# Kernel optimization log

Hardware: AMD Instinct MI355X
Metric: run time of the kernel (lower is better)

Reference implementation:

```python
import jax, jax.numpy as jnp
from jax import lax
import numpy as np

B = 65536
DIM_OBS = 9
DIM_ACT = 4
H = 192
DN = ('NCHW', 'OIHW', 'NCHW')


def _conv(x, w, stride):
    return lax.conv_general_dilated(x, w, (stride, stride), 'VALID', dimension_numbers=DN)


def setup_inputs() -> dict:
    key = jax.random.key(0)
    ks = jax.random.split(key, 16)
    n = lambda k, shp, s: (jax.random.normal(k, shp, dtype=jnp.float32) * s)
    inp = {
        'x': n(ks[0], (B, 1, 12, 16), 1.0),
        'v': n(ks[1], (B, DIM_OBS), 1.0),
        'hx': n(ks[2], (B, H), 1.0),
        # stem convs (no bias)
        'w1': n(ks[3], (32, 1, 2, 2), 0.5),
        'w2': n(ks[4], (64, 32, 3, 3), 0.06),
        'w3': n(ks[5], (128, 64, 3, 3), 0.04),
        'w_stem': n(ks[6], (H, 128 * 2 * 4), 0.03),   # Linear(1024, 192, bias=False)
        # v_proj (weight scaled by 0.5 as in __init__)
        'w_vproj': n(ks[7], (H, DIM_OBS), 0.5 / np.sqrt(DIM_OBS)),
        'b_vproj': n(ks[8], (H,), 0.1),
        # GRUCell(192, 192): gate order r, z, n
        'w_ih': n(ks[9], (3 * H, H), 1.0 / np.sqrt(H)),
        'w_hh': n(ks[10], (3 * H, H), 1.0 / np.sqrt(H)),
        'b_ih': n(ks[11], (3 * H,), 0.05),
        'b_hh': n(ks[12], (3 * H,), 0.05),
        # fc (weight scaled by 0.01 as in __init__)
        'w_fc': n(ks[13], (DIM_ACT, H), 0.01 / np.sqrt(H)),
    }
    return inp


def reference(x, v, hx, w1, w2, w3, w_stem, w_vproj, b_vproj,
              w_ih, w_hh, b_ih, b_hh, w_fc):
    lrelu = lambda t: jax.nn.leaky_relu(t, 0.05)
    # vision stem: [B,1,12,16] -> [B,32,6,8] -> [B,64,4,6] -> [B,128,2,4]
    h = lrelu(_conv(x, w1, 2))
    h = lrelu(_conv(h, w2, 1))
    h = lrelu(_conv(h, w3, 1))
    img_feat = h.reshape(h.shape[0], -1) @ w_stem.T          # [B,192]
    state_feat = v @ w_vproj.T + b_vproj                      # [B,192]
    fused = lrelu(img_feat + state_feat)
    # GRUCell (torch gate order: r, z, n)
    gi = fused @ w_ih.T + b_ih                                # [B,576]
    gh = hx @ w_hh.T + b_hh                                   # [B,576]
    ir, iz, i_n = jnp.split(gi, 3, axis=-1)
    hr, hz, h_n = jnp.split(gh, 3, axis=-1)
    r = jax.nn.sigmoid(ir + hr)
    z = jax.nn.sigmoid(iz + hz)
    n = jnp.tanh(i_n + r * h_n)
    hx_new = (1.0 - z) * n + z * hx
    act = lrelu(hx_new) @ w_fc.T                              # [B,4]
    return act, hx_new
```

## Files before the change

### kernel.cpp

```cpp
#include <hip/hip_runtime.h>


typedef short bf8 __attribute__((ext_vector_type(8)));
typedef float f4  __attribute__((ext_vector_type(4)));

#define MFMA(a, b, c) __builtin_amdgcn_mfma_f32_16x16x32_bf16(a, b, c, 0, 0, 0)

#define W3_OFF    18432
#define WSTEM_OFF 92160
#define WIH_OFF   294912
#define WHH_OFF   405504
#define W_TOTAL   516096
#define C3_OFF    (1 << 20)
#define C2Q_OFF   68157440

__device__ __forceinline__ unsigned short f2bf(float f) {
    unsigned int u = __float_as_uint(f);
    u += 0x7fffu + ((u >> 16) & 1u);
    return (unsigned short)(u >> 16);
}
__device__ __forceinline__ float bf2f(unsigned short h) {
    return __uint_as_float(((unsigned int)h) << 16);
}
__device__ __forceinline__ float lrelu(float v) { return v > 0.f ? v : 0.05f * v; }
__device__ __forceinline__ float sigm(float x) { return 1.f / (1.f + __expf(-x)); }
__device__ __forceinline__ float tanh_(float x) {
    float e = __expf(2.f * x);
    return 1.f - 2.f / (e + 1.f);
}

__global__ void prep_weights(const float* __restrict__ w2, const float* __restrict__ w3,
                             const float* __restrict__ wstem, const float* __restrict__ wvp,
                             const float* __restrict__ wih, const float* __restrict__ whh,
                             unsigned short* __restrict__ o) {
    int i = blockIdx.x * 256 + threadIdx.x;
    if (i >= W_TOTAL) return;
    float val;
    if (i < W3_OFF) {
        int n = i / 288, k = i - n * 288;
        val = w2[n * 288 + (k & 31) * 9 + (k >> 5)];
    } else if (i < WSTEM_OFF) {
        int d = i - W3_OFF;
        int n = d / 576, k = d - n * 576;
        val = w3[n * 576 + (k & 63) * 9 + (k >> 6)];
    } else if (i < WIH_OFF) {
        int d = i - WSTEM_OFF;
        int n = d / 1056, k = d - n * 1056;
        if (k < 1024)       val = wstem[(n << 10) + (k & 127) * 8 + (k >> 7)];
        else if (k < 1033)  val = wvp[n * 9 + (k - 1024)];
        else                val = 0.f;
    } else if (i < WHH_OFF) {
        val = wih[i - WIH_OFF];
    } else {
        val = whh[i - WHH_OFF];
    }
    o[i] = f2bf(val);
}

__global__ __launch_bounds__(256, 2) void conv12(
    const float* __restrict__ x, const float* __restrict__ w1,
    const unsigned short* __restrict__ ws, unsigned short* __restrict__ c2q,
    int sbase)
{
    __shared__ __align__(16) unsigned short lds[6144];
    const int tid = threadIdx.x;
    const int wave = tid >> 6, lane = tid & 63;
    const int col = lane & 15, quad = lane >> 4;
    const int W0 = blockIdx.x * 32;

    bf8 Bf2[9];
    int kq2[9];
    #pragma unroll
    for (int ks = 0; ks < 9; ++ks) {
        int k0 = ks * 32 + quad * 8;
        Bf2[ks] = *(const bf8*)(ws + (wave * 16 + col) * 288 + k0);
        int ky = k0 / 96, r = k0 - 96 * ky;
        kq2[ks] = (ky * 8 + (r >> 5)) * 32 + (r & 31);
    }
    const int g = wave * 2 + (col >> 3);

    for (int c = 0; c < 8; ++c) {
        if (tid < 192) {
            int s = tid / 48, p = tid - s * 48;
            int y = p >> 3, xx = p & 7;
            const float* xp = x + (size_t)(sbase + W0 + c * 4 + s) * 192 + y * 32 + xx * 2;
            float x00 = xp[0], x01 = xp[1], x10 = xp[16], x11 = xp[17];
            int base = s * 1536, sw = (s & 3) << 3;
            #pragma unroll
            for (int cc = 0; cc < 32; ++cc) {
                int co = (cc + p) & 31;
                float a = x00 * w1[co * 4] + x01 * w1[co * 4 + 1]
                        + x10 * w1[co * 4 + 2] + x11 * w1[co * 4 + 3];
                lds[base + ((p * 32 + co) ^ sw)] = f2bf(lrelu(a));
            }
        }
        __syncthreads();

        #pragma unroll
        for (int mt2 = 0; mt2 < 3; ++mt2) {
            int m0 = mt2 * 32 + col, m1 = m0 + 16;
            int s0 = m0 & 3, p0 = m0 >> 2;
            int s1 = m1 & 3, p1 = m1 >> 2;
            int oy0 = p0 / 6, ox0 = p0 - 6 * oy0;
            int oy1 = p1 / 6, ox1 = p1 - 6 * oy1;
            int b0 = s0 * 1536, qb0 = (oy0 * 8 + ox0) * 32, sw0 = (s0 & 3) << 3;
            int b1 = s1 * 1536, qb1 = (oy1 * 8 + ox1) * 32, sw1 = (s1 & 3) << 3;
            f4 acc0 = {0.f, 0.f, 0.f, 0.f}, acc1 = {0.f, 0.f, 0.f, 0.f};
            #pragma unroll
            for (int ks = 0; ks < 9; ++ks) {
                bf8 a0 = *(const bf8*)&lds[b0 + ((qb0 + kq2[ks]) ^ sw0)];
                bf8 a1 = *(const bf8*)&lds[b1 + ((qb1 + kq2[ks]) ^ sw1)];
                acc0 = MFMA(a0, Bf2[ks], acc0);
                acc1 = MFMA(a1, Bf2[ks], acc1);
            }
            #pragma unroll
            for (int r = 0; r < 4; ++r) {
                int m = mt2 * 32 + quad * 4 + r;
                int s = m & 3, pos = m >> 2;
                int sloc = W0 + c * 4 + s;
                int key = (pos + ((sloc & 1) << 2)) & 7;
                c2q[(size_t)sloc * 1536 + pos * 64 + ((g ^ key) << 3) + (col & 7)]
                    = f2bf(lrelu(acc0[r]));
                m += 16; s = m & 3; pos = m >> 2;
                sloc = W0 + c * 4 + s;
                key = (pos + ((sloc & 1) << 2)) & 7;
                c2q[(size_t)sloc * 1536 + pos * 64 + ((g ^ key) << 3) + (col & 7)]
                    = f2bf(lrelu(acc1[r]));
            }
        }
        __syncthreads();
    }
}

__global__ __launch_bounds__(256, 2) void conv3k(
    const unsigned short* __restrict__ ws, const unsigned short* __restrict__ c2q,
    unsigned short* __restrict__ c3, int sbase)
{
    __shared__ __align__(16) unsigned short lds[12288];
    const int tid = threadIdx.x;
    const int wave = tid >> 6, lane = tid & 63;
    const int col = lane & 15, quad = lane >> 4;
    const int h = blockIdx.x & 1;
    const int Q0 = (blockIdx.x >> 1) * 64;
    const int n_in = h * 64 + wave * 16 + col;

    bf8 Bf3[18];
    #pragma unroll
    for (int ks = 0; ks < 18; ++ks)
        Bf3[ks] = *(const bf8*)(ws + W3_OFF + n_in * 576 + ks * 32 + quad * 8);

    int aoff[18];
    {
        int opos = col & 7;
        int oy = opos >> 2, ox = opos & 3;
        int spar = (col >> 3) & 1;
        #pragma unroll
        for (int ks = 0; ks < 18; ++ks) {
            int k0 = ks * 32 + quad * 8;
            int b = k0 >> 6;
            int ky = b / 3, kx = b - 3 * ky;
            int pos2 = (oy + ky) * 6 + (ox + kx);
            int gg = (k0 & 63) >> 3;
            int key = (pos2 + (spar << 2)) & 7;
            aoff[ks] = pos2 * 64 + ((gg ^ key) << 3);
        }
    }
    const int Gl = h * 8 + wave * 2 + (col >> 3);

    for (int c = 0; c < 8; ++c) {
        const unsigned short* s2 = c2q + (size_t)(Q0 + c * 8) * 1536 + tid * 48;
        #pragma unroll
        for (int i = 0; i < 6; ++i)
            *(bf8*)&lds[tid * 48 + i * 8] = *(const bf8*)(s2 + i * 8);
        __syncthreads();

        f4 acc[4];
        #pragma unroll
        for (int mt = 0; mt < 4; ++mt) acc[mt] = (f4){0.f, 0.f, 0.f, 0.f};
        #pragma unroll
        for (int ks = 0; ks < 18; ++ks) {
            #pragma unroll
            for (int mt = 0; mt < 4; ++mt) {
                int sc = mt * 2 + (col >> 3);
                bf8 a = *(const bf8*)&lds[sc * 1536 + aoff[ks]];
                acc[mt] = MFMA(a, Bf3[ks], acc[mt]);
            }
        }
        #pragma unroll
        for (int mt = 0; mt < 4; ++mt) {
            #pragma unroll
            for (int r = 0; r < 4; ++r) {
                int m = quad * 4 + r;
                int sc = mt * 2 + (m >> 3), opos = m & 7;
                int srow = sbase + Q0 + c * 8 + sc;
                c3[(size_t)srow * 1024 + opos * 128 + ((Gl ^ (srow & 15)) << 3) + (col & 7)]
                    = f2bf(lrelu(acc[mt][r]));
            }
        }
        __syncthreads();
    }
}

__global__ __launch_bounds__(256, 2) void stem_gru(
    const unsigned short* __restrict__ ws, const float* __restrict__ v,
    const float* __restrict__ hx, const float* __restrict__ bvp,
    const float* __restrict__ bih, const float* __restrict__ bhh,
    const float* __restrict__ wfc, float* __restrict__ out)
{
    __shared__ __align__(16) unsigned short lds[28672];
    const int tid = threadIdx.x;
    const int wave = tid >> 6, lane = tid & 63;
    const int col = lane & 15, quad = lane >> 4;
    const int S0 = blockIdx.x * 64;
    const unsigned short* c3 = ws + C3_OFF;
    const unsigned short* wstem = ws + WSTEM_OFF;

    f4 acc[4][3];
    #pragma unroll
    for (int mt = 0; mt < 4; ++mt)
        #pragma unroll
        for (int t = 0; t < 3; ++t) acc[mt][t] = (f4){0.f, 0.f, 0.f, 0.f};

    const int sm = tid >> 2, sq = tid & 3;
    const unsigned short* asrc = c3 + (size_t)(S0 + sm) * 1024 + sq * 32;

    #pragma unroll
    for (int i = 0; i < 4; ++i)
        *(bf8*)&lds[12288 + sm * 128 + sq * 32 + i * 8] = *(const bf8*)(asrc + i * 8);
    __syncthreads();

    for (int kc = 0; kc < 8; ++kc) {
        bf8 nx[4];
        if (kc < 7) {
            const unsigned short* s2 = asrc + (kc + 1) * 128;
            #pragma unroll
            for (int i = 0; i < 4; ++i) nx[i] = *(const bf8*)(s2 + i * 8);
        }
        int abase = 12288 + (kc & 1) * 8192;
        #pragma unroll
        for (int ks = 0; ks < 4; ++ks) {
            int kl = ks * 32 + quad * 8;
            int kk = kc * 128 + kl;
            bf8 b0 = *(const bf8*)(wstem + (wave * 48 + col) * 1056 + kk);
            bf8 b1 = *(const bf8*)(wstem + (wave * 48 + 16 + col) * 1056 + kk);
            bf8 b2 = *(const bf8*)(wstem + (wave * 48 + 32 + col) * 1056 + kk);
            #pragma unroll
            for (int mt = 0; mt < 4; ++mt) {
                int m = mt * 16 + col;
                bf8 a = *(const bf8*)&lds[abase + m * 128 + (kl ^ ((m & 15) << 3))];
                acc[mt][0] = MFMA(a, b0, acc[mt][0]);
                acc[mt][1] = MFMA(a, b1, acc[mt][1]);
                acc[mt][2] = MFMA(a, b2, acc[mt][2]);
            }
        }
        if (kc < 7) {
            int wb = 12288 + ((kc + 1) & 1) * 8192;
            #pragma unroll
            for (int i = 0; i < 4; ++i)
                *(bf8*)&lds[wb + sm * 128 + sq * 32 + i * 8] = nx[i];
        }
        __syncthreads();
    }

    if (tid < 64) {
        int m = tid;
        const float* vp = v + (size_t)(S0 + m) * 9;
        __align__(16) unsigned short tmp[32];
        #pragma unroll
        for (int i = 0; i < 9; ++i) tmp[i] = f2bf(vp[i]);
        #pragma unroll
        for (int i = 9; i < 32; ++i) tmp[i] = 0;
        #pragma unroll
        for (int gg = 0; gg < 4; ++gg) {
            int gp = gg ^ (m & 15);
            *(bf8*)&lds[12288 + m * 128 + gp * 8] = *(bf8*)&tmp[gg * 8];
        }
    }
    __syncthreads();
    {
        int kl = quad * 8;
        bf8 b0 = *(const bf8*)(wstem + (wave * 48 + col) * 1056 + 1024 + kl);
        bf8 b1 = *(const bf8*)(wstem + (wave * 48 + 16 + col) * 1056 + 1024 + kl);
        bf8 b2 = *(const bf8*)(wstem + (wave * 48 + 32 + col) * 1056 + 1024 + kl);
        #pragma unroll
        for (int mt = 0; mt < 4; ++mt) {
            int m = mt * 16 + col;
            bf8 a = *(const bf8*)&lds[12288 + m * 128 + (kl ^ ((m & 15) << 3))];
            acc[mt][0] = MFMA(a, b0, acc[mt][0]);
            acc[mt][1] = MFMA(a, b1, acc[mt][1]);
            acc[mt][2] = MFMA(a, b2, acc[mt][2]);
        }
    }

    #pragma unroll
    for (int t = 0; t < 3; ++t) {
        int n = wave * 48 + t * 16 + col;
        float bb = bvp[n];
        #pragma unroll
        for (int mt = 0; mt < 4; ++mt)
            #pragma unroll
            for (int r = 0; r < 4; ++r) {
                int m = mt * 16 + quad * 4 + r;
                lds[m * 192 + (n ^ ((m & 7) << 3))] = f2bf(lrelu(acc[mt][t][r] + bb));
            }
    }
    __syncthreads();

    {
        int m = tid >> 2, qq = tid & 3;
        const float* hp = hx + (size_t)(S0 + m) * 192 + qq * 48;
        #pragma unroll
        for (int i = 0; i < 6; ++i) {
            f4 d = *(const f4*)(hp + i * 8 + 0);
            f4 d2 = *(const f4*)(hp + i * 8 + 4);
            __align__(16) unsigned short tmp[8];
            #pragma unroll
            for (int u = 0; u < 4; ++u) { tmp[u] = f2bf(d[u]); tmp[4 + u] = f2bf(d2[u]); }
            int gg = qq * 6 + i, gp = gg ^ (m & 7);
            *(bf8*)&lds[12288 + m * 192 + gp * 8] = *(bf8*)tmp;
        }
    }
    __syncthreads();

    #pragma unroll
    for (int t = 0; t < 3; ++t) {
        int j0 = (wave * 3 + t) * 16;
        int j = j0 + col;
        const unsigned short* pih = ws + WIH_OFF + j * 192;
        const unsigned short* phh = ws + WHH_OFF + j * 192;
        f4 g0[4], g1[4], g2[4], g3[4], g4[4], g5[4];
        #pragma unroll
        for (int mt = 0; mt < 4; ++mt) {
            g0[mt] = (f4){0.f,0.f,0.f,0.f}; g1[mt] = g0[mt]; g2[mt] = g0[mt];
            g3[mt] = g0[mt]; g4[mt] = g0[mt]; g5[mt] = g0[mt];
        }
        #pragma unroll
        for (int ks = 0; ks < 6; ++ks) {
            int k0 = ks * 32 + quad * 8;
            bf8 bir = *(const bf8*)(pih + k0);
            bf8 bhr = *(const bf8*)(phh + k0);
            bf8 biz = *(const bf8*)(pih + 36864 + k0);
            bf8 bhz = *(const bf8*)(phh + 36864 + k0);
            bf8 bin = *(const bf8*)(pih + 73728 + k0);
            bf8 bhn = *(const bf8*)(phh + 73728 + k0);
            #pragma unroll
            for (int mt = 0; mt < 4; ++mt) {
                int m = mt * 16 + col;
                int off = m * 192 + (k0 ^ ((m & 7) << 3));
                bf8 aF = *(const bf8*)&lds[off];
                bf8 aH = *(const bf8*)&lds[12288 + off];
                g0[mt] = MFMA(aF, bir, g0[mt]);
                g1[mt] = MFMA(aH, bhr, g1[mt]);
                g2[mt] = MFMA(aF, biz, g2[mt]);
                g3[mt] = MFMA(aH, bhz, g3[mt]);
                g4[mt] = MFMA(aF, bin, g4[mt]);
                g5[mt] = MFMA(aH, bhn, g5[mt]);
            }
        }
        float b_ir = bih[j], b_iz = bih[192 + j], b_in = bih[384 + j];
        float b_hr = bhh[j], b_hz = bhh[192 + j], b_hn = bhh[384 + j];
        #pragma unroll
        for (int mt = 0; mt < 4; ++mt)
            #pragma unroll
            for (int r = 0; r < 4; ++r) {
                int s = mt * 16 + quad * 4 + r;
                float rg = sigm(g0[mt][r] + b_ir + g1[mt][r] + b_hr);
                float zg = sigm(g2[mt][r] + b_iz + g3[mt][r] + b_hz);
                float ng = tanh_(g4[mt][r] + b_in + rg * (g5[mt][r] + b_hn));
                float hxv = hx[(size_t)(S0 + s) * 192 + j];
                float hnew = (1.f - zg) * ng + zg * hxv;
                out[65536 * 4 + (size_t)(S0 + s) * 192 + j] = hnew;
            }
    }
    __syncthreads();

    {
        int s = tid & 63, a = tid >> 6;
        const float* hp = out + 65536 * 4 + (size_t)(S0 + s) * 192;
        const float* wf = wfc + a * 192;
        float sum = 0.f;
        #pragma unroll 4
        for (int jj = 0; jj < 48; ++jj) {
            f4 hv = *(const f4*)(hp + jj * 4);
            f4 wv = *(const f4*)(wf + jj * 4);
            #pragma unroll
            for (int u = 0; u < 4; ++u) sum += lrelu(hv[u]) * wv[u];
        }
        out[(size_t)(S0 + s) * 4 + a] = sum;
    }
}

extern "C" void kernel_launch(void* const* d_in, const int* in_sizes, int n_in,
                              void* d_out, int out_size, void* d_ws, size_t ws_size,
                              hipStream_t stream) {
    const float* x     = (const float*)d_in[0];
    const float* v     = (const float*)d_in[1];
    const float* hx    = (const float*)d_in[2];
    const float* w1    = (const float*)d_in[3];
    const float* w2    = (const float*)d_in[4];
    const float* w3    = (const float*)d_in[5];
    const float* wstem = (const float*)d_in[6];
    const float* wvp   = (const float*)d_in[7];
    const float* bvp   = (const float*)d_in[8];
    const float* wih   = (const float*)d_in[9];
    const float* whh   = (const float*)d_in[10];
    const float* bih   = (const float*)d_in[11];
    const float* bhh   = (const float*)d_in[12];
    const float* wfc   = (const float*)d_in[13];
    unsigned short* wsp = (unsigned short*)d_ws;
    unsigned short* c3  = wsp + C3_OFF;
    unsigned short* c2q = wsp + C2Q_OFF;

    prep_weights<<<2016, 256, 0, stream>>>(w2, w3, wstem, wvp, wih, whh, wsp);
    for (int q = 0; q < 4; ++q) {
        conv12<<<512, 256, 0, stream>>>(x, w1, wsp, c2q, q * 16384);
        conv3k<<<512, 256, 0, stream>>>(wsp, c2q, c3, q * 16384);
    }
    stem_gru<<<1024, 256, 0, stream>>>(wsp, v, hx, bvp, bih, bhh, wfc, (float*)d_out);
}
```

Before: 581.7 us.

## Fuse conv1/conv2/conv3 into one kernel keeping conv2 output in LDS

Merges the conv12 and conv3k kernels into a single convfused kernel. conv2 activations stay in shared memory instead of making a round trip through a global c2q buffer, and the four-way batch-chunked launch loop is removed. Each block handles one output-channel half of conv3, so conv1 and conv2 are computed twice (once by each half-block pair) in exchange for skipping the intermediate global write and read. Separately, stem_gru drops its double-buffered LDS staging to a single buffer with extra barriers so it can raise launch bounds to 3 blocks per CU.

```diff
diff --git a/kernel.cpp b/kernel.cpp
--- a/kernel.cpp
+++ b/kernel.cpp
@@ -12,21 +12,20 @@
 #define WHH_OFF   405504
 #define W_TOTAL   516096
 #define C3_OFF    (1 << 20)
-#define C2Q_OFF   68157440
 
 __device__ __forceinline__ unsigned short f2bf(float f) {
     unsigned int u = __float_as_uint(f);
     u += 0x7fffu + ((u >> 16) & 1u);
     return (unsigned short)(u >> 16);
-}
-__device__ __forceinline__ float bf2f(unsigned short h) {
-    return __uint_as_float(((unsigned int)h) << 16);
 }
 __device__ __forceinline__ float lrelu(float v) { return v > 0.f ? v : 0.05f * v; }
 __device__ __forceinline__ float sigm(float x) { return 1.f / (1.f + __expf(-x)); }
 __device__ __forceinline__ float tanh_(float x) {
     float e = __expf(2.f * x);
     return 1.f - 2.f / (e + 1.f);
+}
+__device__ __forceinline__ int swzC(int q, int s) {
+    return q ^ ((s & 3) << 3) ^ ((q >> 1) & 32);
 }
 
 __global__ void prep_weights(const float* __restrict__ w2, const float* __restrict__ w3,
@@ -57,33 +56,58 @@
     o[i] = f2bf(val);
 }
 
-__global__ __launch_bounds__(256, 2) void conv12(
+__global__ __launch_bounds__(256, 2) void convfused(
     const float* __restrict__ x, const float* __restrict__ w1,
-    const unsigned short* __restrict__ ws, unsigned short* __restrict__ c2q,
-    int sbase)
+    const unsigned short* __restrict__ ws, unsigned short* __restrict__ c3)
 {
-    __shared__ __align__(16) unsigned short lds[6144];
+    __shared__ __align__(16) unsigned short lds[31232];
     const int tid = threadIdx.x;
     const int wave = tid >> 6, lane = tid & 63;
     const int col = lane & 15, quad = lane >> 4;
-    const int W0 = blockIdx.x * 32;
-
-    bf8 Bf2[9];
-    int kq2[9];
-    #pragma unroll
-    for (int ks = 0; ks < 9; ++ks) {
-        int k0 = ks * 32 + quad * 8;
-        Bf2[ks] = *(const bf8*)(ws + (wave * 16 + col) * 288 + k0);
-        int ky = k0 / 96, r = k0 - 96 * ky;
-        kq2[ks] = (ky * 8 + (r >> 5)) * 32 + (r & 31);
-    }
-    const int g = wave * 2 + (col >> 3);
-
-    for (int c = 0; c < 8; ++c) {
+    const int h = blockIdx.x & 1;
+    const int S0 = (blockIdx.x >> 1) * 64;
+    const int q8 = quad * 8;
+
+    {
+        int row = tid >> 2, seg = tid & 3;
+        const unsigned short* src = ws + row * 288 + seg * 72;
+        unsigned short* dst = &lds[12288 + row * 296 + seg * 72];
+        #pragma unroll
+        for (int i = 0; i < 9; ++i)
+            *(bf8*)(dst + i * 8) = *(const bf8*)(src + i * 8);
+    }
+
+    const int n_in = h * 64 + wave * 16 + col;
+    bf8 Bf3[18];
+    #pragma unroll
+    for (int ks = 0; ks < 18; ++ks)
+        Bf3[ks] = *(const bf8*)(ws + W3_OFF + n_in * 576 + ks * 32 + q8);
+
+    const int scm = col & 3;
+    const int bb2 = scm * 1536, sw2 = scm << 3;
+    int qbv[6];
+    #pragma unroll
+    for (int mt = 0; mt < 3; ++mt)
+        #pragma unroll
+        for (int hf = 0; hf < 2; ++hf) {
+            int p = mt * 8 + hf * 4 + (col >> 2);
+            int oy = p / 6, ox = p - 6 * oy;
+            qbv[mt * 2 + hf] = (oy * 8 + ox) * 32;
+        }
+    const int s3 = col & 3;
+    const int p30 = col >> 2, p31 = p30 + 4;
+    const int qb30 = p30 * 64;
+    const int qb31 = (6 + (p31 & 3)) * 64;
+    const int b3 = 6144 + s3 * 1536;
+    const int G = h * 8 + wave * 2 + (col >> 3);
+
+    __syncthreads();
+
+    for (int c = 0; c < 16; ++c) {
         if (tid < 192) {
             int s = tid / 48, p = tid - s * 48;
             int y = p >> 3, xx = p & 7;
-            const float* xp = x + (size_t)(sbase + W0 + c * 4 + s) * 192 + y * 32 + xx * 2;
+            const float* xp = x + (size_t)(S0 + c * 4 + s) * 192 + y * 32 + xx * 2;
             float x00 = xp[0], x01 = xp[1], x10 = xp[16], x11 = xp[17];
             int base = s * 1536, sw = (s & 3) << 3;
             #pragma unroll
@@ -96,118 +120,69 @@
         }
         __syncthreads();
 
-        #pragma unroll
-        for (int mt2 = 0; mt2 < 3; ++mt2) {
-            int m0 = mt2 * 32 + col, m1 = m0 + 16;
-            int s0 = m0 & 3, p0 = m0 >> 2;
-            int s1 = m1 & 3, p1 = m1 >> 2;
-            int oy0 = p0 / 6, ox0 = p0 - 6 * oy0;
-            int oy1 = p1 / 6, ox1 = p1 - 6 * oy1;
-            int b0 = s0 * 1536, qb0 = (oy0 * 8 + ox0) * 32, sw0 = (s0 & 3) << 3;
-            int b1 = s1 * 1536, qb1 = (oy1 * 8 + ox1) * 32, sw1 = (s1 & 3) << 3;
-            f4 acc0 = {0.f, 0.f, 0.f, 0.f}, acc1 = {0.f, 0.f, 0.f, 0.f};
+        {
+            f4 a2[6];
+            #pragma unroll
+            for (int i = 0; i < 6; ++i) a2[i] = (f4){0.f, 0.f, 0.f, 0.f};
+            const int brow = 12288 + (wave * 16 + col) * 296;
             #pragma unroll
             for (int ks = 0; ks < 9; ++ks) {
-                bf8 a0 = *(const bf8*)&lds[b0 + ((qb0 + kq2[ks]) ^ sw0)];
-                bf8 a1 = *(const bf8*)&lds[b1 + ((qb1 + kq2[ks]) ^ sw1)];
-                acc0 = MFMA(a0, Bf2[ks], acc0);
-                acc1 = MFMA(a1, Bf2[ks], acc1);
+                bf8 b = *(const bf8*)&lds[brow + ks * 32 + q8];
+                const int kqc = ((ks / 3) * 8 + (ks % 3)) * 32 + q8;
+                #pragma unroll
+                for (int i = 0; i < 6; ++i) {
+                    bf8 a = *(const bf8*)&lds[bb2 + ((qbv[i] + kqc) ^ sw2)];
+                    a2[i] = MFMA(a, b, a2[i]);
+                }
+            }
+            #pragma unroll
+            for (int mt = 0; mt < 3; ++mt)
+                #pragma unroll
+                for (int hf = 0; hf < 2; ++hf) {
+                    f4 ac = a2[mt * 2 + hf];
+                    #pragma unroll
+                    for (int r = 0; r < 4; ++r) {
+                        int m = mt * 32 + hf * 16 + quad * 4 + r;
+                        int s = m & 3, pos = m >> 2;
+                        int q = pos * 64 + wave * 16 + col;
+                        lds[6144 + s * 1536 + swzC(q, s)] = f2bf(lrelu(ac[r]));
+                    }
+                }
+        }
+        __syncthreads();
+
+        {
+            f4 a30 = {0.f, 0.f, 0.f, 0.f}, a31 = {0.f, 0.f, 0.f, 0.f};
+            #pragma unroll
+            for (int ks = 0; ks < 18; ++ks) {
+                const int kqc = ((ks / 6) * 6 + ((ks % 6) >> 1)) * 64
+                              + ((ks % 6) & 1) * 32 + q8;
+                bf8 x0 = *(const bf8*)&lds[b3 + swzC(qb30 + kqc, s3)];
+                bf8 x1 = *(const bf8*)&lds[b3 + swzC(qb31 + kqc, s3)];
+                a30 = MFMA(x0, Bf3[ks], a30);
+                a31 = MFMA(x1, Bf3[ks], a31);
             }
             #pragma unroll
             for (int r = 0; r < 4; ++r) {
-                int m = mt2 * 32 + quad * 4 + r;
-                int s = m & 3, pos = m >> 2;
-                int sloc = W0 + c * 4 + s;
-                int key = (pos + ((sloc & 1) << 2)) & 7;
-                c2q[(size_t)sloc * 1536 + pos * 64 + ((g ^ key) << 3) + (col & 7)]
-                    = f2bf(lrelu(acc0[r]));
-                m += 16; s = m & 3; pos = m >> 2;
-                sloc = W0 + c * 4 + s;
-                key = (pos + ((sloc & 1) << 2)) & 7;
-                c2q[(size_t)sloc * 1536 + pos * 64 + ((g ^ key) << 3) + (col & 7)]
-                    = f2bf(lrelu(acc1[r]));
-            }
-        }
-        __syncthreads();
-    }
-}
-
-__global__ __launch_bounds__(256, 2) void conv3k(
-    const unsigned short* __restrict__ ws, const unsigned short* __restrict__ c2q,
-    unsigned short* __restrict__ c3, int sbase)
-{
-    __shared__ __align__(16) unsigned short lds[12288];
-    const int tid = threadIdx.x;
-    const int wave = tid >> 6, lane = tid & 63;
-    const int col = lane & 15, quad = lane >> 4;
-    const int h = blockIdx.x & 1;
-    const int Q0 = (blockIdx.x >> 1) * 64;
-    const int n_in = h * 64 + wave * 16 + col;
-
-    bf8 Bf3[18];
-    #pragma unroll
-    for (int ks = 0; ks < 18; ++ks)
-        Bf3[ks] = *(const bf8*)(ws + W3_OFF + n_in * 576 + ks * 32 + quad * 8);
-
-    int aoff[18];
-    {
-        int opos = col & 7;
-        int oy = opos >> 2, ox = opos & 3;
-        int spar = (col >> 3) & 1;
-        #pragma unroll
-        for (int ks = 0; ks < 18; ++ks) {
-            int k0 = ks * 32 + quad * 8;
-            int b = k0 >> 6;
-            int ky = b / 3, kx = b - 3 * ky;
-            int pos2 = (oy + ky) * 6 + (ox + kx);
-            int gg = (k0 & 63) >> 3;
-            int key = (pos2 + (spar << 2)) & 7;
-            aoff[ks] = pos2 * 64 + ((gg ^ key) << 3);
-        }
-    }
-    const int Gl = h * 8 + wave * 2 + (col >> 3);
-
-    for (int c = 0; c < 8; ++c) {
-        const unsigned short* s2 = c2q + (size_t)(Q0 + c * 8) * 1536 + tid * 48;
-        #pragma unroll
-        for (int i = 0; i < 6; ++i)
-            *(bf8*)&lds[tid * 48 + i * 8] = *(const bf8*)(s2 + i * 8);
-        __syncthreads();
-
-        f4 acc[4];
-        #pragma unroll
-        for (int mt = 0; mt < 4; ++mt) acc[mt] = (f4){0.f, 0.f, 0.f, 0.f};
-        #pragma unroll
-        for (int ks = 0; ks < 18; ++ks) {
-            #pragma unroll
-            for (int mt = 0; mt < 4; ++mt) {
-                int sc = mt * 2 + (col >> 3);
-                bf8 a = *(const bf8*)&lds[sc * 1536 + aoff[ks]];
-                acc[mt] = MFMA(a, Bf3[ks], acc[mt]);
-            }
-        }
-        #pragma unroll
-        for (int mt = 0; mt < 4; ++mt) {
-            #pragma unroll
-            for (int r = 0; r < 4; ++r) {
-                int m = quad * 4 + r;
-                int sc = mt * 2 + (m >> 3), opos = m & 7;
-                int srow = sbase + Q0 + c * 8 + sc;
-                c3[(size_t)srow * 1024 + opos * 128 + ((Gl ^ (srow & 15)) << 3) + (col & 7)]
-                    = f2bf(lrelu(acc[mt][r]));
-            }
-        }
-        __syncthreads();
-    }
-}
-
-__global__ __launch_bounds__(256, 2) void stem_gru(
+                int srow = S0 + c * 4 + r;
+                int key = (G ^ (srow & 15)) << 3;
+                c3[(size_t)srow * 1024 + quad * 128 + key + (col & 7)]
+                    = f2bf(lrelu(a30[r]));
+                c3[(size_t)srow * 1024 + (quad + 4) * 128 + key + (col & 7)]
+                    = f2bf(lrelu(a31[r]));
+            }
+        }
+        __syncthreads();
+    }
+}
+
+__global__ __launch_bounds__(256, 3) void stem_gru(
     const unsigned short* __restrict__ ws, const float* __restrict__ v,
     const float* __restrict__ hx, const float* __restrict__ bvp,
     const float* __restrict__ bih, const float* __restrict__ bhh,
     const float* __restrict__ wfc, float* __restrict__ out)
 {
-    __shared__ __align__(16) unsigned short lds[28672];
+    __shared__ __align__(16) unsigned short lds[24576];
     const int tid = threadIdx.x;
     const int wave = tid >> 6, lane = tid & 63;
     const int col = lane & 15, quad = lane >> 4;
@@ -236,7 +211,6 @@
             #pragma unroll
             for (int i = 0; i < 4; ++i) nx[i] = *(const bf8*)(s2 + i * 8);
         }
-        int abase = 12288 + (kc & 1) * 8192;
         #pragma unroll
         for (int ks = 0; ks < 4; ++ks) {
             int kl = ks * 32 + quad * 8;
@@ -247,17 +221,17 @@
             #pragma unroll
             for (int mt = 0; mt < 4; ++mt) {
                 int m = mt * 16 + col;
-                bf8 a = *(const bf8*)&lds[abase + m * 128 + (kl ^ ((m & 15) << 3))];
+                bf8 a = *(const bf8*)&lds[12288 + m * 128 + (kl ^ ((m & 15) << 3))];
                 acc[mt][0] = MFMA(a, b0, acc[mt][0]);
                 acc[mt][1] = MFMA(a, b1, acc[mt][1]);
                 acc[mt][2] = MFMA(a, b2, acc[mt][2]);
             }
         }
+        __syncthreads();
         if (kc < 7) {
-            int wb = 12288 + ((kc + 1) & 1) * 8192;
             #pragma unroll
             for (int i = 0; i < 4; ++i)
-                *(bf8*)&lds[wb + sm * 128 + sq * 32 + i * 8] = nx[i];
+                *(bf8*)&lds[12288 + sm * 128 + sq * 32 + i * 8] = nx[i];
         }
         __syncthreads();
     }
@@ -291,6 +265,7 @@
             acc[mt][2] = MFMA(a, b2, acc[mt][2]);
         }
     }
+    __syncthreads();
 
     #pragma unroll
     for (int t = 0; t < 3; ++t) {
@@ -304,14 +279,13 @@
                 lds[m * 192 + (n ^ ((m & 7) << 3))] = f2bf(lrelu(acc[mt][t][r] + bb));
             }
     }
-    __syncthreads();
 
     {
         int m = tid >> 2, qq = tid & 3;
         const float* hp = hx + (size_t)(S0 + m) * 192 + qq * 48;
         #pragma unroll
         for (int i = 0; i < 6; ++i) {
-            f4 d = *(const f4*)(hp + i * 8 + 0);
+            f4 d  = *(const f4*)(hp + i * 8 + 0);
             f4 d2 = *(const f4*)(hp + i * 8 + 4);
             __align__(16) unsigned short tmp[8];
             #pragma unroll
@@ -369,14 +343,14 @@
                 float ng = tanh_(g4[mt][r] + b_in + rg * (g5[mt][r] + b_hn));
                 float hxv = hx[(size_t)(S0 + s) * 192 + j];
                 float hnew = (1.f - zg) * ng + zg * hxv;
-                out[65536 * 4 + (size_t)(S0 + s) * 192 + j] = hnew;
+                out[262144 + (size_t)(S0 + s) * 192 + j] = hnew;
             }
     }
     __syncthreads();
 
     {
         int s = tid & 63, a = tid >> 6;
-        const float* hp = out + 65536 * 4 + (size_t)(S0 + s) * 192;
+        const float* hp = out + 262144 + (size_t)(S0 + s) * 192;
         const float* wf = wfc + a * 192;
         float sum = 0.f;
         #pragma unroll 4
@@ -408,13 +382,8 @@
     const float* bhh   = (const float*)d_in[12];
     const float* wfc   = (const float*)d_in[13];
     unsigned short* wsp = (unsigned short*)d_ws;
-    unsigned short* c3  = wsp + C3_OFF;
-    unsigned short* c2q = wsp + C2Q_OFF;
 
     prep_weights<<<2016, 256, 0, stream>>>(w2, w3, wstem, wvp, wih, whh, wsp);
-    for (int q = 0; q < 4; ++q) {
-        conv12<<<512, 256, 0, stream>>>(x, w1, wsp, c2q, q * 16384);
-        conv3k<<<512, 256, 0, stream>>>(wsp, c2q, c3, q * 16384);
-    }
+    convfused<<<2048, 256, 0, stream>>>(x, w1, wsp, wsp + C3_OFF);
     stem_gru<<<1024, 256, 0, stream>>>(wsp, v, hx, bvp, bih, bhh, wfc, (float*)d_out);
 }
```

Result: slower. 1.820 ms (+212.8%).
